# Kernel tuning notes

Hardware: AMD Instinct MI355X
Metric: run time of the kernel (lower is better)

The kernel has to match this reference:

```python
import jax, jax.numpy as jnp
import numpy as np

IMG = 512      # diffusion image side
CUT_SIZE = 224 # CLIP input resolution
CUTN = 64
CUT_POW = 1.0


def setup_inputs() -> dict:
    key = jax.random.key(0)
    k1, k2, k3, k4 = jax.random.split(key, 4)
    B, C, H, W = 4, 3, IMG, IMG
    x = jax.random.normal(k1, (B, C, H, W), dtype=jnp.float32)
    max_size = min(H, W)
    min_size = min(H, W, CUT_SIZE)
    # size = int(rand()**cut_pow * (max_size - min_size) + min_size)
    u = jax.random.uniform(k2, (CUTN,))
    sizes = ((u ** CUT_POW) * (max_size - min_size) + min_size).astype(jnp.int32)
    # offsets uniform in [0, side - size]
    offsetx = (jax.random.uniform(k3, (CUTN,)) * (W - sizes + 1).astype(jnp.float32)).astype(jnp.int32)
    offsety = (jax.random.uniform(k4, (CUTN,)) * (H - sizes + 1).astype(jnp.float32)).astype(jnp.int32)
    return {"x": x, "sizes": sizes, "offsetx": offsetx, "offsety": offsety, "cut_size": CUT_SIZE}


def _make_cutouts(x, sizes, offsetx, offsety, S):
    # Fused batched crop + bilinear resize (torch F.interpolate, align_corners=False).
    B, C, H, W = x.shape
    N = sizes.shape[0]
    sizes_f = sizes.astype(x.dtype)
    # source coords within the crop: (j + 0.5) * size/S - 0.5, clamped at 0
    grid = jnp.arange(S, dtype=x.dtype) + 0.5                      # [S]
    src = jnp.maximum(sizes_f[:, None] / S * grid[None, :] - 0.5, 0.0)  # [N,S]
    i0 = jnp.floor(src).astype(jnp.int32)
    frac = src - i0.astype(x.dtype)                                # [N,S]
    i0 = jnp.minimum(i0, sizes[:, None] - 1)
    i1 = jnp.minimum(i0 + 1, sizes[:, None] - 1)
    # global indices into the full image (crops are square: same grid for y and x)
    Y0 = (offsety[:, None] + i0)[:, :, None]  # [N,S,1]
    Y1 = (offsety[:, None] + i1)[:, :, None]
    X0 = (offsetx[:, None] + i0)[:, None, :]  # [N,1,S]
    X1 = (offsetx[:, None] + i1)[:, None, :]
    wy = frac[:, :, None]                      # [N,S,1]
    wx = frac[:, None, :]                      # [N,1,S]
    # four-corner gather: each is [B,C,N,S,S]
    v00 = x[:, :, Y0, X0]
    v01 = x[:, :, Y0, X1]
    v10 = x[:, :, Y1, X0]
    v11 = x[:, :, Y1, X1]
    out = (v00 * (1 - wy) * (1 - wx) + v01 * (1 - wy) * wx
           + v10 * wy * (1 - wx) + v11 * wy * wx)
    # torch.cat over cutouts -> cutout-major: [N*B, C, S, S]
    return out.transpose(2, 0, 1, 3, 4).reshape(N * B, C, S, S)


def reference(x, sizes, offsetx, offsety, cut_size):
    return _make_cutouts(x, sizes, offsetx, offsety, cut_size)
```

## Files before the change

kernel.cpp:

```cpp
#include <hip/hip_runtime.h>
#include <stdint.h>

constexpr int S   = 224;
constexpr int Wim = 512;
constexpr int Him = 512;
constexpr int PLANES = 12;
constexpr int N   = 64;
constexpr int SB  = 16;
constexpr int NBANDS = Him / SB;
constexpr int NGRP = 8;
constexpr int GROUPS = N / NGRP;
constexpr int TILES = PLANES * NBANDS;
constexpr int TPX   = TILES / 8;
constexpr int WPB   = 4;
constexpr int GRID  = TILES * GROUPS;
constexpr int ROWF  = 516;

__device__ __forceinline__ void load_lds16(const float* g, float* l) {
    __builtin_amdgcn_global_load_lds(
        (const __attribute__((address_space(1))) void*)g,
        (__attribute__((address_space(3))) void*)l, 16, 0, 0);
}

__device__ __forceinline__ int iy0_of(int i, float scale, int sz) {
    const float sy = fmaxf(scale * ((float)i + 0.5f) - 0.5f, 0.0f);
    return min((int)floorf(sy), sz - 1);
}

__global__ __launch_bounds__(256) void cutouts_kernel(
    const float* __restrict__ x,
    const int*   __restrict__ sizes,
    const int*   __restrict__ offx,
    const int*   __restrict__ offy,
    float*       __restrict__ out)
{
    __shared__ float lds[SB + 1][ROWF];

    const int lane = threadIdx.x & 63;
    const int wv   = threadIdx.x >> 6;

    const int xcd   = blockIdx.x & 7;
    const int local = blockIdx.x >> 3;
    const int tk    = local >> 3;
    const int g     = local & 7;
    const int t     = xcd * TPX + tk;
    const int pi    = t >> 5;
    const int b     = t & 31;

    if (threadIdx.x < (SB + 1) * 4)
        lds[threadIdx.x >> 2][Wim + (threadIdx.x & 3)] = 0.0f;

    const float* plane = x + (size_t)pi * (Him * Wim);
    for (int c = wv; c < (SB + 1) * 2; c += WPB) {
        const int row  = c >> 1, half = c & 1;
        const int srow = min(SB * b + row, Him - 1);
        load_lds16(plane + (size_t)srow * Wim + half * 256 + lane * 4,
                   &lds[row][half * 256]);
    }

    int flv;
    {
        const int   idx = lane & 7;
        const int   nn_ = g * NGRP + idx;
        const int   szl = sizes[nn_];
        const int   oyl = offy[nn_];
        const float scl = (float)szl / (float)S;
        const int   P   = SB * b - oyl + ((lane & 8) ? SB : 0);
        int res;
        if (P <= 0) res = 0;
        else if (P > szl - 1) res = S;
        else {
            const float cc = ((float)P + 0.5f) / scl - 0.5f;
            int i = (int)ceilf(fminf(fmaxf(cc, 0.0f), (float)S));
            while (i > 0 && iy0_of(i - 1, scl, szl) >= P) --i;
            while (i < S && iy0_of(i, scl, szl) < P) ++i;
            res = i;
        }
        flv = res;
    }

    asm volatile("s_waitcnt vmcnt(0)" ::: "memory");
    __syncthreads();

    #pragma unroll 1
    for (int nn = 0; nn < NGRP; ++nn) {
        const int i_lo = __builtin_amdgcn_readlane(flv, nn);
        const int i_hi = __builtin_amdgcn_readlane(flv, nn + 8);
        if (i_lo >= i_hi) continue;

        const int n  = g * NGRP + nn;
        const int sz = sizes[n];
        const int oy = offy[n];
        const int ox = offx[n];
        const float scale = (float)sz / (float)S;
        const int   L     = SB * b - oy;

        int dv[4]; float fxv[4];
        #pragma unroll
        for (int r = 0; r < 4; ++r) {
            const int   px = r * 64 + lane;
            const float sx = fmaxf(scale * ((float)px + 0.5f) - 0.5f, 0.0f);
            const float fi = floorf(sx);
            fxv[r] = sx - fi;
            dv[r]  = ox + (int)fi;
        }

        float* oplane = out + (size_t)(n * PLANES + pi) * (S * S);

        for (int i = i_lo + wv; i < i_hi; i += WPB) {
            const float sy  = fmaxf(scale * ((float)i + 0.5f) - 0.5f, 0.0f);
            const float fiy = floorf(sy);
            const float fy  = sy - fiy;
            const int   rel = (int)fiy - L;
            const float* l0 = &lds[rel][0];
            const float* l1 = &lds[rel + 1][0];
            float* orow = oplane + (size_t)i * S;

            #pragma unroll
            for (int r = 0; r < 4; ++r) {
                if (r < 3 || lane < 32) {
                    const int   d = dv[r];
                    const float f = fxv[r];
                    const float a0 = l0[d], a1 = l0[d + 1];
                    const float c0 = l1[d], c1 = l1[d + 1];
                    const float top = a0 + (a1 - a0) * f;
                    const float bot = c0 + (c1 - c0) * f;
                    orow[r * 64 + lane] = top + (bot - top) * fy;
                }
            }
        }
    }
}

extern "C" void kernel_launch(void* const* d_in, const int* in_sizes, int n_in,
                              void* d_out, int out_size, void* d_ws, size_t ws_size,
                              hipStream_t stream) {
    const float* x     = (const float*)d_in[0];
    const int*   sizes = (const int*)d_in[1];
    const int*   offx  = (const int*)d_in[2];
    const int*   offy  = (const int*)d_in[3];
    float* out = (float*)d_out;

    cutouts_kernel<<<GRID, 256, 0, stream>>>(x, sizes, offx, offy, out);
}
```

Baseline: 39.48 us.

## Stage source rows in LDS as packed fp16 horizontal pairs

New measurement: 41.52 us. +5.2%, slower.

```diff
diff --git a/kernel.cpp b/kernel.cpp
--- a/kernel.cpp
+++ b/kernel.cpp
@@ -1,4 +1,5 @@
 #include <hip/hip_runtime.h>
+#include <hip/hip_fp16.h>
 #include <stdint.h>
 
 constexpr int S   = 224;
@@ -14,13 +15,11 @@
 constexpr int TPX   = TILES / 8;
 constexpr int WPB   = 4;
 constexpr int GRID  = TILES * GROUPS;
-constexpr int ROWF  = 516;
+constexpr int ROWP  = 516;
 
-__device__ __forceinline__ void load_lds16(const float* g, float* l) {
-    __builtin_amdgcn_global_load_lds(
-        (const __attribute__((address_space(1))) void*)g,
-        (__attribute__((address_space(3))) void*)l, 16, 0, 0);
-}
+typedef float    f32x4 __attribute__((ext_vector_type(4)));
+typedef _Float16 f16x2 __attribute__((ext_vector_type(2)));
+typedef uint32_t u32x4 __attribute__((ext_vector_type(4)));
 
 __device__ __forceinline__ int iy0_of(int i, float scale, int sz) {
     const float sy = fmaxf(scale * ((float)i + 0.5f) - 0.5f, 0.0f);
@@ -34,7 +33,7 @@
     const int*   __restrict__ offy,
     float*       __restrict__ out)
 {
-    __shared__ float lds[SB + 1][ROWF];
+    __shared__ uint32_t pb[SB + 1][ROWP];
 
     const int lane = threadIdx.x & 63;
     const int wv   = threadIdx.x >> 6;
@@ -47,15 +46,29 @@
     const int pi    = t >> 5;
     const int b     = t & 31;
 
-    if (threadIdx.x < (SB + 1) * 4)
-        lds[threadIdx.x >> 2][Wim + (threadIdx.x & 3)] = 0.0f;
+    const float* plane = x + (size_t)pi * (Him * Wim);
 
-    const float* plane = x + (size_t)pi * (Him * Wim);
-    for (int c = wv; c < (SB + 1) * 2; c += WPB) {
+    f32x4 sv[9]; float se[9];
+    #pragma unroll
+    for (int k = 0; k < 9; ++k) {
+        const int c    = min(wv + 4 * k, 33);
         const int row  = c >> 1, half = c & 1;
         const int srow = min(SB * b + row, Him - 1);
-        load_lds16(plane + (size_t)srow * Wim + half * 256 + lane * 4,
-                   &lds[row][half * 256]);
+        const int c0   = half * 256 + 4 * lane;
+        const float* rp = plane + (size_t)srow * Wim + c0;
+        sv[k] = *(const f32x4*)rp;
+        se[k] = plane[(size_t)srow * Wim + min(c0 + 4, Wim - 1)];
+    }
+    #pragma unroll
+    for (int k = 0; k < 9; ++k) {
+        const int c   = min(wv + 4 * k, 33);
+        const int row = c >> 1, half = c & 1;
+        u32x4 w;
+        w.x = __builtin_bit_cast(uint32_t, __builtin_amdgcn_cvt_pkrtz(sv[k].x, sv[k].y));
+        w.y = __builtin_bit_cast(uint32_t, __builtin_amdgcn_cvt_pkrtz(sv[k].y, sv[k].z));
+        w.z = __builtin_bit_cast(uint32_t, __builtin_amdgcn_cvt_pkrtz(sv[k].z, sv[k].w));
+        w.w = __builtin_bit_cast(uint32_t, __builtin_amdgcn_cvt_pkrtz(sv[k].w, se[k]));
+        *(u32x4*)&pb[row][half * 256 + 4 * lane] = w;
     }
 
     int flv;
@@ -79,7 +92,6 @@
         flv = res;
     }
 
-    asm volatile("s_waitcnt vmcnt(0)" ::: "memory");
     __syncthreads();
 
     #pragma unroll 1
@@ -112,19 +124,22 @@
             const float fiy = floorf(sy);
             const float fy  = sy - fiy;
             const int   rel = (int)fiy - L;
-            const float* l0 = &lds[rel][0];
-            const float* l1 = &lds[rel + 1][0];
+            const uint32_t* r0 = &pb[rel][0];
             float* orow = oplane + (size_t)i * S;
 
             #pragma unroll
             for (int r = 0; r < 4; ++r) {
                 if (r < 3 || lane < 32) {
-                    const int   d = dv[r];
-                    const float f = fxv[r];
-                    const float a0 = l0[d], a1 = l0[d + 1];
-                    const float c0 = l1[d], c1 = l1[d + 1];
-                    const float top = a0 + (a1 - a0) * f;
-                    const float bot = c0 + (c1 - c0) * f;
+                    const int d  = dv[r];
+                    const uint32_t u0 = r0[d];
+                    const uint32_t u1 = r0[d + ROWP];
+                    const f16x2 a = __builtin_bit_cast(f16x2, u0);
+                    const f16x2 c = __builtin_bit_cast(f16x2, u1);
+                    const float ax = (float)a.x, ay = (float)a.y;
+                    const float cx = (float)c.x, cy = (float)c.y;
+                    const float f  = fxv[r];
+                    const float top = ax + (ay - ax) * f;
+                    const float bot = cx + (cy - cx) * f;
                     orow[r * 64 + lane] = top + (bot - top) * fy;
                 }
             }
```
